# Kernel optimization log

Hardware: AMD Instinct MI355X
Metric: run time of the kernel (lower is better)

The kernel has to match this reference:

```python
import jax, jax.numpy as jnp
import numpy as np

NODE_DIM = 256
OUTPUT_DIM = 256
NUM_HOPS = 4
NUM_NODES = 25000
NUM_EDGES = 400000
NUM_TYPES = 10
FEAT_DIM = 32


def setup_inputs() -> dict:
    key = jax.random.key(0)
    ks = jax.random.split(key, 12)
    nodes = jax.random.normal(ks[0], (NUM_NODES, FEAT_DIM), dtype=jnp.float32)
    edges = jax.random.randint(ks[1], (2, NUM_EDGES), 0, NUM_NODES, dtype=jnp.int64)
    node_types = jax.random.randint(ks[2], (NUM_NODES,), 0, NUM_TYPES, dtype=jnp.int64)
    s = 0.02
    type_emb = jax.random.normal(ks[3], (NUM_TYPES, NODE_DIM), dtype=jnp.float32) * s
    W_proj = jax.random.normal(ks[4], (FEAT_DIM, NODE_DIM), dtype=jnp.float32) * s
    b_proj = jnp.zeros((NODE_DIM,), dtype=jnp.float32)
    W_msg = jax.random.normal(ks[5], (NUM_HOPS, 2 * NODE_DIM, NODE_DIM), dtype=jnp.float32) * s
    b_msg = jnp.zeros((NUM_HOPS, NODE_DIM), dtype=jnp.float32)
    W_upd = jax.random.normal(ks[6], (NUM_HOPS, 2 * NODE_DIM, NODE_DIM), dtype=jnp.float32) * s
    b_upd = jnp.zeros((NUM_HOPS, NODE_DIM), dtype=jnp.float32)
    W_out = jax.random.normal(ks[7], (NODE_DIM, OUTPUT_DIM), dtype=jnp.float32) * s
    b_out = jnp.zeros((OUTPUT_DIM,), dtype=jnp.float32)
    return {"nodes": nodes, "edges": edges, "node_types": node_types,
            "type_emb": type_emb, "W_proj": W_proj, "b_proj": b_proj,
            "W_msg": W_msg, "b_msg": b_msg, "W_upd": W_upd, "b_upd": b_upd,
            "W_out": W_out, "b_out": b_out}


def reference(nodes, edges, node_types, type_emb, W_proj, b_proj,
              W_msg, b_msg, W_upd, b_upd, W_out, b_out):
    n = nodes.shape[0]
    src, dst = edges[0], edges[1]
    # initial node states: linear proj + type embedding
    h = nodes @ W_proj + b_proj + type_emb[node_types]  # [N, D]
    for i in range(NUM_HOPS):
        edge_feat = jnp.concatenate([h[src], h[dst]], axis=1)      # [E, 2D]
        messages = edge_feat @ W_msg[i] + b_msg[i]                 # [E, D]
        agg = jax.ops.segment_sum(messages, dst, num_segments=n)   # [N, D]
        h = jax.nn.relu(jnp.concatenate([h, agg], axis=1) @ W_upd[i] + b_upd[i])
    graph_embedding = jnp.max(h, axis=0)                           # [D]
    return graph_embedding @ W_out + b_out                          # [output_dim]
```

## Files before the change

kernel.cpp:

```cpp
#include <hip/hip_runtime.h>
#include <hip/hip_bf16.h>

#define NDIM 256
#define FDIM 32
#define HOPS 4
#define NPB 8

typedef __attribute__((ext_vector_type(8))) short short8;
typedef __attribute__((ext_vector_type(4))) float f32x4;
typedef __attribute__((ext_vector_type(2))) float f32x2;

__device__ inline float b2f(unsigned short u) {
    union { unsigned int i; float f; } v; v.i = ((unsigned int)u) << 16; return v.f;
}
__device__ inline unsigned short f2b(float f) {
    union { float f; unsigned int i; } v; v.f = f;
    unsigned int r = v.i + 0x7FFF + ((v.i >> 16) & 1);
    return (unsigned short)(r >> 16);
}
__device__ inline unsigned char f2fp8(float v) {
    return (unsigned char)(__builtin_amdgcn_cvt_pk_fp8_f32(v, v, 0, false) & 0xFF);
}

__global__ __launch_bounds__(256) void prep_mega_kernel(
        const int* __restrict__ dst, int* __restrict__ deg, int E, int histB,
        const float* __restrict__ Wm, const float* __restrict__ Wu,
        const float* __restrict__ bm,
        unsigned short* __restrict__ WtA, unsigned short* __restrict__ WtB,
        unsigned short* __restrict__ WtC,
        float* __restrict__ cvec, int* __restrict__ geInt,
        unsigned char* __restrict__ h8row,
        const float* __restrict__ nodes, const int* __restrict__ node_types,
        const float* __restrict__ type_emb, const float* __restrict__ W_proj,
        const float* __restrict__ b_proj,
        unsigned short* __restrict__ h, unsigned char* __restrict__ h8, int n) {
    __shared__ float T[32][33];
    __shared__ float Af[32][68];
    __shared__ float Bf[32][68];
    __shared__ float sb[256];
    int b = blockIdx.x;
    int t = threadIdx.x;

    if (b < histB) {
        int e = b * 256 + t;
        if (e < E) atomicAdd(&deg[dst[e]], 1);
    } else if (b < histB + 389) {
        int bb = b - histB;
        if (bb < 256) {
            int hop = bb >> 6;
            int rem = bb & 63;
            int k0 = (rem & 7) * 32, n0 = (rem >> 3) * 32;
            const float* src = Wu + (size_t)hop * 512 * 256;
            unsigned short* dstp = WtB + (size_t)hop * 256 * 256;
            int tr = t >> 5, tc = t & 31;
#pragma unroll
            for (int r = 0; r < 4; ++r) {
                int k = tr + r * 8;
                T[tc][k] = src[(size_t)(k0 + k) * 256 + n0 + tc];
            }
            __syncthreads();
#pragma unroll
            for (int r = 0; r < 4; ++r) {
                int nn = tr + r * 8;
                dstp[(size_t)(n0 + nn) * 256 + k0 + tc] = f2b(T[nn][tc]);
            }
        } else if (bb < 384) {
            int idx = bb - 256;
            int m = idx >> 4;
            int rem = idx & 15;
            int k0 = (rem & 3) * 64, n0 = (rem >> 2) * 64;
            int hop = m >> 1, which = m & 1;
            const float* A = Wm + (size_t)hop * 512 * 256 + (size_t)which * 256 * 256;
            const float* B = Wu + (size_t)hop * 512 * 256 + (size_t)256 * 256;
            unsigned short* W = (which ? WtC : WtA) + (size_t)hop * 256 * 256;
            int tx = t & 15, ty = t >> 4;
            float acc[4][4];
#pragma unroll
            for (int a = 0; a < 4; ++a)
#pragma unroll
                for (int c = 0; c < 4; ++c) acc[a][c] = 0.f;

            for (int j0 = 0; j0 < 256; j0 += 32) {
                __syncthreads();
#pragma unroll
                for (int c = 0; c < 2; ++c) {
                    int idx2 = t + c * 256;
                    int kk = idx2 >> 3;
                    int jj = (idx2 & 7) * 4;
                    float4 va = *(const float4*)&A[(size_t)(k0 + kk) * 256 + j0 + jj];
                    Af[jj + 0][kk] = va.x; Af[jj + 1][kk] = va.y;
                    Af[jj + 2][kk] = va.z; Af[jj + 3][kk] = va.w;
                    int jj2 = idx2 >> 4;
                    int nn = (idx2 & 15) * 4;
                    float4 vb = *(const float4*)&B[(size_t)(j0 + jj2) * 256 + n0 + nn];
                    *(float4*)&Bf[jj2][nn] = vb;
                }
                __syncthreads();
#pragma unroll
                for (int jj = 0; jj < 32; ++jj) {
                    float av[4];
#pragma unroll
                    for (int a = 0; a < 4; ++a) av[a] = Af[jj][ty * 4 + a];
                    float4 bv = *(const float4*)&Bf[jj][tx * 4];
#pragma unroll
                    for (int a = 0; a < 4; ++a) {
                        acc[a][0] += av[a] * bv.x; acc[a][1] += av[a] * bv.y;
                        acc[a][2] += av[a] * bv.z; acc[a][3] += av[a] * bv.w;
                    }
                }
            }
#pragma unroll
            for (int c = 0; c < 4; ++c) {
                int nn = n0 + tx * 4 + c;
                ushort4 o;
                o.x = f2b(acc[0][c]); o.y = f2b(acc[1][c]);
                o.z = f2b(acc[2][c]); o.w = f2b(acc[3][c]);
                *(ushort4*)&W[(size_t)nn * 256 + k0 + ty * 4] = o;
            }
        } else if (bb < 388) {
            int hop = bb - 384;
            sb[t] = bm[hop * 256 + t];
            __syncthreads();
            const float* B = Wu + (size_t)hop * 512 * 256 + (size_t)256 * 256;
            float acc = 0.f;
#pragma unroll 8
            for (int j = 0; j < 256; ++j) acc += sb[j] * B[(size_t)j * 256 + t];
            cvec[hop * 256 + t] = acc;
        } else {
            geInt[t] = 0;
            h8row[t] = 0;
        }
    } else {
        int v0 = (b - histB - 389) * NPB;
        {
            int j = t >> 5, f = t & 31;
            int v = v0 + j;
            sb[t] = (v < n) ? nodes[(size_t)v * FDIM + f] : 0.f;
        }
        __syncthreads();
        float acc[NPB];
#pragma unroll
        for (int j = 0; j < NPB; ++j) {
            int v = v0 + j;
            acc[j] = (v < n) ? (b_proj[t] + type_emb[(size_t)node_types[v] * NDIM + t]) : 0.f;
        }
#pragma unroll 4
        for (int k = 0; k < FDIM; ++k) {
            float wv = W_proj[(size_t)k * NDIM + t];
#pragma unroll
            for (int j = 0; j < NPB; ++j)
                acc[j] += sb[j * FDIM + k] * wv;
        }
#pragma unroll
        for (int j = 0; j < NPB; ++j) {
            int v = v0 + j;
            if (v < n) {
                h[(size_t)v * NDIM + t] = f2b(acc[j]);
                h8[(size_t)v * NDIM + t] = f2fp8(acc[j]);
            }
        }
    }
}

__global__ __launch_bounds__(1024) void scan_kernel(const int* __restrict__ deg,
                                                    int* __restrict__ rowptr,
                                                    int* __restrict__ cursor, int n) {
    __shared__ int wsum[16];
    int t = threadIdx.x;
    int per4 = (n + 4095) >> 12;
    int base = t * per4 * 4;
    int4 v4[8];
#pragma unroll 8
    for (int j = 0; j < per4; ++j) {
        int4 d = *(const int4*)(deg + base + j * 4);
        d.x = (d.x + 7) & ~7; d.y = (d.y + 7) & ~7;
        d.z = (d.z + 7) & ~7; d.w = (d.w + 7) & ~7;
        v4[j] = d;
    }
    int s = 0;
#pragma unroll 8
    for (int j = 0; j < per4; ++j) s += v4[j].x + v4[j].y + v4[j].z + v4[j].w;

    int lane = t & 63, wid = t >> 6;
    int v = s;
#pragma unroll
    for (int d = 1; d < 64; d <<= 1) {
        int u = __shfl_up(v, d, 64);
        if (lane >= d) v += u;
    }
    if (lane == 63) wsum[wid] = v;
    __syncthreads();
    if (wid == 0) {
        int ws = (lane < 16) ? wsum[lane] : 0;
#pragma unroll
        for (int d = 1; d < 16; d <<= 1) {
            int u = __shfl_up(ws, d, 64);
            if (lane >= d) ws += u;
        }
        if (lane < 16) wsum[lane] = ws;
    }
    __syncthreads();
    int run = (wid > 0 ? wsum[wid - 1] : 0) + (v - s);
#pragma unroll 8
    for (int j = 0; j < per4; ++j) {
        int idx = base + j * 4;
        int4 o;
        o.x = run; run += v4[j].x;
        o.y = run; run += v4[j].y;
        o.z = run; run += v4[j].z;
        o.w = run; run += v4[j].w;
        if (idx + 3 < n) {
            *(int4*)(rowptr + idx) = o;
            *(int4*)(cursor + idx) = o;
        } else if (idx < n) {
            const int* op = (const int*)&o;
            for (int e = 0; e < 4 && idx + e < n; ++e) {
                rowptr[idx + e] = op[e];
                cursor[idx + e] = op[e];
            }
        }
    }
    if (t == 1023) rowptr[n] = run;
}

__global__ void fillpad_kernel(const int* __restrict__ src, const int* __restrict__ dst,
                               int* __restrict__ cursor,
                               const int* __restrict__ rowptr, const int* __restrict__ deg,
                               int* __restrict__ col, int E, int fillB, int n) {
    int b = blockIdx.x;
    int t = threadIdx.x;
    if (b < fillB) {
        int e = b * 256 + t;
        if (e < E) {
            int d = dst[e];
            int p = atomicAdd(&cursor[d], 1);
            col[p] = src[e];
        }
    } else {
        int v = (b - fillB) * 256 + t;
        if (v < n) {
            int s = rowptr[v] + deg[v];
            int e0 = rowptr[v + 1];
            for (int i = s; i < e0; ++i) col[i] = n;
        }
    }
}

__global__ __launch_bounds__(256) void agg_kernel(const unsigned char* __restrict__ h8,
                                                  const int* __restrict__ rowptr,
                                                  const int* __restrict__ col,
                                                  unsigned short* __restrict__ S, int n) {
    int wave = threadIdx.x >> 6;
    int lane = threadIdx.x & 63;
    int half = lane >> 5;
    int hl = lane & 31;
    int v = blockIdx.x * 8 + wave * 2 + half;
    if (v >= n) return;
    int beg = rowptr[v], end = rowptr[v + 1];
    float a[8];
#pragma unroll
    for (int e = 0; e < 8; ++e) a[e] = 0.f;
    int cofs = hl * 8;
    for (int i = beg; i < end; i += 8) {
        int cc[8];
#pragma unroll
        for (int j = 0; j < 8; ++j) cc[j] = col[i + j];
        uint2 x[8];
#pragma unroll
        for (int j = 0; j < 8; ++j)
            x[j] = *(const uint2*)(h8 + (size_t)cc[j] * NDIM + cofs);
#pragma unroll
        for (int j = 0; j < 8; ++j) {
            f32x2 p0 = __builtin_amdgcn_cvt_pk_f32_fp8(x[j].x, false);
            f32x2 p1 = __builtin_amdgcn_cvt_pk_f32_fp8(x[j].x, true);
            f32x2 p2 = __builtin_amdgcn_cvt_pk_f32_fp8(x[j].y, false);
            f32x2 p3 = __builtin_amdgcn_cvt_pk_f32_fp8(x[j].y, true);
            a[0] += p0[0]; a[1] += p0[1]; a[2] += p1[0]; a[3] += p1[1];
            a[4] += p2[0]; a[5] += p2[1]; a[6] += p3[0]; a[7] += p3[1];
        }
    }
    uint4 o;
    unsigned short* op = (unsigned short*)&o;
#pragma unroll
    for (int e = 0; e < 8; ++e) op[e] = f2b(a[e]);
    *(uint4*)&S[(size_t)v * NDIM + cofs] = o;
}

#define BM 128
#define BN 64
#define BK 64
#define ASTR (BK + 8)

template <bool LAST>
__global__ __launch_bounds__(256) void gemm_hop_kernel(const unsigned short* __restrict__ S,
                                                       const unsigned short* __restrict__ hcur,
                                                       const int* __restrict__ deg,
                                                       const unsigned short* __restrict__ WtA,
                                                       const unsigned short* __restrict__ WtB,
                                                       const unsigned short* __restrict__ WtC,
                                                       const float* __restrict__ bupd,
                                                       const float* __restrict__ cvec,
                                                       unsigned short* __restrict__ Out,
                                                       unsigned char* __restrict__ Out8,
                                                       int* __restrict__ geInt, int n) {
    __shared__ unsigned short As[BM][ASTR];
    __shared__ unsigned short Bs[BN][ASTR];
    __shared__ unsigned short Cs[BN][ASTR];
    __shared__ int smax[BN];
    int t = threadIdx.x;
    int lane = t & 63;
    int w = t >> 6;
    int wm = w >> 1, wn = w & 1;
    int quad = lane >> 4, l16 = lane & 15;
    int row0 = blockIdx.x * BM;
    int n0 = blockIdx.y * BN;

    if (LAST) {
        if (t < BN) smax[t] = 0;
    }

    f32x4 acc1[4][2], acc2[4][2];
#pragma unroll
    for (int i = 0; i < 4; ++i)
#pragma unroll
        for (int j = 0; j < 2; ++j) { acc1[i][j] = (f32x4)(0.f); acc2[i][j] = (f32x4)(0.f); }

    for (int k0 = 0; k0 < NDIM; k0 += BK) {
        __syncthreads();
#pragma unroll
        for (int h2 = 0; h2 < 4; ++h2) {
            int c = t + h2 * 256;
            int r = c >> 3;
            int ko = (c & 7) * 8;
            int grow = row0 + r; if (grow >= n) grow = n - 1;
            *(uint4*)&As[r][ko] = *(const uint4*)(S + (size_t)grow * NDIM + k0 + ko);
        }
#pragma unroll
        for (int h2 = 0; h2 < 2; ++h2) {
            int c = t + h2 * 256;
            int r = c >> 3;
            int ko = (c & 7) * 8;
            *(uint4*)&Bs[r][ko] = *(const uint4*)(WtA + (size_t)(n0 + r) * NDIM + k0 + ko);
        }
        __syncthreads();
#pragma unroll
        for (int ks = 0; ks < BK; ks += 32) {
            short8 af[4], bf[2];
#pragma unroll
            for (int mt = 0; mt < 4; ++mt)
                af[mt] = *(const short8*)&As[wm * 64 + mt * 16 + l16][ks + quad * 8];
#pragma unroll
            for (int nt = 0; nt < 2; ++nt)
                bf[nt] = *(const short8*)&Bs[wn * 32 + nt * 16 + l16][ks + quad * 8];
#pragma unroll
            for (int mt = 0; mt < 4; ++mt)
#pragma unroll
                for (int nt = 0; nt < 2; ++nt)
                    acc1[mt][nt] = __builtin_amdgcn_mfma_f32_16x16x32_bf16(af[mt], bf[nt], acc1[mt][nt], 0, 0, 0);
        }
    }
    for (int k0 = 0; k0 < NDIM; k0 += BK) {
        __syncthreads();
#pragma unroll
        for (int h2 = 0; h2 < 4; ++h2) {
            int c = t + h2 * 256;
            int r = c >> 3;
            int ko = (c & 7) * 8;
            int grow = row0 + r; if (grow >= n) grow = n - 1;
            *(uint4*)&As[r][ko] = *(const uint4*)(hcur + (size_t)grow * NDIM + k0 + ko);
        }
#pragma unroll
        for (int h2 = 0; h2 < 2; ++h2) {
            int c = t + h2 * 256;
            int r = c >> 3;
            int ko = (c & 7) * 8;
            size_t widx = (size_t)(n0 + r) * NDIM + k0 + ko;
            *(uint4*)&Bs[r][ko] = *(const uint4*)(WtB + widx);
            *(uint4*)&Cs[r][ko] = *(const uint4*)(WtC + widx);
        }
        __syncthreads();
#pragma unroll
        for (int ks = 0; ks < BK; ks += 32) {
            short8 af[4], bf[2], cf[2];
#pragma unroll
            for (int mt = 0; mt < 4; ++mt)
                af[mt] = *(const short8*)&As[wm * 64 + mt * 16 + l16][ks + quad * 8];
#pragma unroll
            for (int nt = 0; nt < 2; ++nt) {
                bf[nt] = *(const short8*)&Bs[wn * 32 + nt * 16 + l16][ks + quad * 8];
                cf[nt] = *(const short8*)&Cs[wn * 32 + nt * 16 + l16][ks + quad * 8];
            }
#pragma unroll
            for (int mt = 0; mt < 4; ++mt)
#pragma unroll
                for (int nt = 0; nt < 2; ++nt) {
                    acc1[mt][nt] = __builtin_amdgcn_mfma_f32_16x16x32_bf16(af[mt], bf[nt], acc1[mt][nt], 0, 0, 0);
                    acc2[mt][nt] = __builtin_amdgcn_mfma_f32_16x16x32_bf16(af[mt], cf[nt], acc2[mt][nt], 0, 0, 0);
                }
        }
    }
#pragma unroll
    for (int mt = 0; mt < 4; ++mt) {
#pragma unroll
        for (int nt = 0; nt < 2; ++nt) {
            int lcol = wn * 32 + nt * 16 + l16;
            int col = n0 + lcol;
            float bu = bupd[col];
            float cv = cvec[col];
            float cmax = 0.f;
#pragma unroll
            for (int r = 0; r < 4; ++r) {
                int row = row0 + wm * 64 + mt * 16 + quad * 4 + r;
                if (row < n) {
                    float dg = (float)deg[row];
                    float v = fmaxf(acc1[mt][nt][r] + dg * (acc2[mt][nt][r] + cv) + bu, 0.f);
                    Out[(size_t)row * NDIM + col] = f2b(v);
                    if (!LAST) Out8[(size_t)row * NDIM + col] = f2fp8(v);
                    if (LAST) cmax = fmaxf(cmax, v);
                }
            }
            if (LAST) atomicMax(&smax[lcol], __float_as_int(cmax));
        }
    }
    if (LAST) {
        __syncthreads();
        if (t < BN) atomicMax(&geInt[n0 + t], smax[t]);
    }
}

__global__ __launch_bounds__(1024) void out_kernel(const float* __restrict__ ge,
                                                   const float* __restrict__ W_out,
                                                   const float* __restrict__ b_out,
                                                   float* __restrict__ out) {
    __shared__ float red[4][NDIM];
    int t = threadIdx.x & 255;
    int g = threadIdx.x >> 8;
    float acc = 0.f;
#pragma unroll 8
    for (int kk = 0; kk < 64; ++kk) {
        int k = g * 64 + kk;
        acc += ge[k] * W_out[k * NDIM + t];
    }
    red[g][t] = acc;
    __syncthreads();
    if (g == 0)
        out[t] = b_out[t] + red[0][t] + red[1][t] + red[2][t] + red[3][t];
}

extern "C" void kernel_launch(void* const* d_in, const int* in_sizes, int n_in,
                              void* d_out, int out_size, void* d_ws, size_t ws_size,
                              hipStream_t stream) {
    const float* nodes      = (const float*)d_in[0];
    const int*   edges      = (const int*)d_in[1];
    const int*   node_types = (const int*)d_in[2];
    const float* type_emb   = (const float*)d_in[3];
    const float* W_proj     = (const float*)d_in[4];
    const float* b_proj     = (const float*)d_in[5];
    const float* W_msg      = (const float*)d_in[6];
    const float* b_msg      = (const float*)d_in[7];
    const float* W_upd      = (const float*)d_in[8];
    const float* b_upd      = (const float*)d_in[9];
    const float* W_out      = (const float*)d_in[10];
    const float* b_out      = (const float*)d_in[11];

    int n = in_sizes[2];
    int E = in_sizes[1] / 2;
    const int* src = edges;
    const int* dst = edges + E;

    size_t off = 0;
    auto alloc = [&](size_t bytes) {
        void* p = (char*)d_ws + off;
        off += (bytes + 255) & ~(size_t)255;
        return p;
    };
    int* deg    = (int*)alloc((size_t)(n + 4096) * 4);
    int* rowptr = (int*)alloc((size_t)(n + 1) * 4);
    int* cursor = (int*)alloc((size_t)n * 4);
    int* col    = (int*)alloc((size_t)(E + 8 * n) * 4);
    unsigned short* WtA = (unsigned short*)alloc((size_t)HOPS * 256 * 256 * 2);
    unsigned short* WtB = (unsigned short*)alloc((size_t)HOPS * 256 * 256 * 2);
    unsigned short* WtC = (unsigned short*)alloc((size_t)HOPS * 256 * 256 * 2);
    float* cvec = (float*)alloc((size_t)HOPS * 256 * 4);
    int* geInt  = (int*)alloc((size_t)256 * 4);
    unsigned short* hA  = (unsigned short*)alloc((size_t)(n + 1) * NDIM * 2);
    unsigned short* hB  = (unsigned short*)alloc((size_t)(n + 1) * NDIM * 2);
    unsigned short* Sb  = (unsigned short*)alloc((size_t)n * NDIM * 2);
    unsigned char* h8   = (unsigned char*)alloc((size_t)(n + 1) * NDIM);

    hipMemsetAsync(deg, 0, (size_t)(n + 4096) * 4, stream);
    int eb = (E + 255) / 256;
    int pb = (n + 255) / 256;
    int ib = (n + NPB - 1) / NPB;
    prep_mega_kernel<<<eb + 389 + ib, 256, 0, stream>>>(
        dst, deg, E, eb,
        W_msg, W_upd, b_msg, WtA, WtB, WtC, cvec, geInt, h8 + (size_t)n * NDIM,
        nodes, node_types, type_emb, W_proj, b_proj, hA, h8, n);
    scan_kernel<<<1, 1024, 0, stream>>>(deg, rowptr, cursor, n);
    fillpad_kernel<<<eb + pb, 256, 0, stream>>>(src, dst, cursor, rowptr, deg, col, E, eb, n);

    unsigned short* h  = hA;
    unsigned short* ho = hB;
    int gx = (n + BM - 1) / BM;
    dim3 ggrid(gx, NDIM / BN);
    for (int i = 0; i < HOPS; ++i) {
        agg_kernel<<<(n + 7) / 8, 256, 0, stream>>>(h8, rowptr, col, Sb, n);
        size_t wofs = (size_t)i * 256 * 256;
        if (i == HOPS - 1)
            gemm_hop_kernel<true><<<ggrid, 256, 0, stream>>>(
                Sb, h, deg, WtA + wofs, WtB + wofs, WtC + wofs,
                b_upd + (size_t)i * NDIM, cvec + (size_t)i * NDIM, ho, h8, geInt, n);
        else
            gemm_hop_kernel<false><<<ggrid, 256, 0, stream>>>(
                Sb, h, deg, WtA + wofs, WtB + wofs, WtC + wofs,
                b_upd + (size_t)i * NDIM, cvec + (size_t)i * NDIM, ho, h8, geInt, n);
        unsigned short* tmp = h; h = ho; ho = tmp;
    }
    out_kernel<<<1, 1024, 0, stream>>>((const float*)geInt, W_out, b_out, (float*)d_out);
}
```

Measured before the change: 365.6 us.

## Move weight-product precompute to MFMA blocks in scan kernel, restructure aggregation

Removes the scalar FP32 tiled matmul that folds W_msg into W_upd from the prep kernel. It is recomputed with bf16 MFMA instructions in extra blocks of the scan kernel, which now launches 9 blocks, so the small weight GEMMs overlap the single-block scan instead of lengthening the prep kernel. The aggregation kernel is also restructured: each quarter-wave handles different neighbors with 16-byte fp8 loads per lane, and the partial sums are reduced with cross-lane shuffles. Converting the weight-product inputs to bf16 before multiplying adds rounding error compared with the FP32 accumulation.

```diff
diff --git a/kernel.cpp b/kernel.cpp
--- a/kernel.cpp
+++ b/kernel.cpp
@@ -24,10 +24,8 @@
 
 __global__ __launch_bounds__(256) void prep_mega_kernel(
         const int* __restrict__ dst, int* __restrict__ deg, int E, int histB,
-        const float* __restrict__ Wm, const float* __restrict__ Wu,
-        const float* __restrict__ bm,
-        unsigned short* __restrict__ WtA, unsigned short* __restrict__ WtB,
-        unsigned short* __restrict__ WtC,
+        const float* __restrict__ Wu, const float* __restrict__ bm,
+        unsigned short* __restrict__ WtB,
         float* __restrict__ cvec, int* __restrict__ geInt,
         unsigned char* __restrict__ h8row,
         const float* __restrict__ nodes, const int* __restrict__ node_types,
@@ -35,8 +33,6 @@
         const float* __restrict__ b_proj,
         unsigned short* __restrict__ h, unsigned char* __restrict__ h8, int n) {
     __shared__ float T[32][33];
-    __shared__ float Af[32][68];
-    __shared__ float Bf[32][68];
     __shared__ float sb[256];
     int b = blockIdx.x;
     int t = threadIdx.x;
@@ -44,7 +40,7 @@
     if (b < histB) {
         int e = b * 256 + t;
         if (e < E) atomicAdd(&deg[dst[e]], 1);
-    } else if (b < histB + 389) {
+    } else if (b < histB + 261) {
         int bb = b - histB;
         if (bb < 256) {
             int hop = bb >> 6;
@@ -64,61 +60,8 @@
                 int nn = tr + r * 8;
                 dstp[(size_t)(n0 + nn) * 256 + k0 + tc] = f2b(T[nn][tc]);
             }
-        } else if (bb < 384) {
-            int idx = bb - 256;
-            int m = idx >> 4;
-            int rem = idx & 15;
-            int k0 = (rem & 3) * 64, n0 = (rem >> 2) * 64;
-            int hop = m >> 1, which = m & 1;
-            const float* A = Wm + (size_t)hop * 512 * 256 + (size_t)which * 256 * 256;
-            const float* B = Wu + (size_t)hop * 512 * 256 + (size_t)256 * 256;
-            unsigned short* W = (which ? WtC : WtA) + (size_t)hop * 256 * 256;
-            int tx = t & 15, ty = t >> 4;
-            float acc[4][4];
-#pragma unroll
-            for (int a = 0; a < 4; ++a)
-#pragma unroll
-                for (int c = 0; c < 4; ++c) acc[a][c] = 0.f;
-
-            for (int j0 = 0; j0 < 256; j0 += 32) {
-                __syncthreads();
-#pragma unroll
-                for (int c = 0; c < 2; ++c) {
-                    int idx2 = t + c * 256;
-                    int kk = idx2 >> 3;
-                    int jj = (idx2 & 7) * 4;
-                    float4 va = *(const float4*)&A[(size_t)(k0 + kk) * 256 + j0 + jj];
-                    Af[jj + 0][kk] = va.x; Af[jj + 1][kk] = va.y;
-                    Af[jj + 2][kk] = va.z; Af[jj + 3][kk] = va.w;
-                    int jj2 = idx2 >> 4;
-                    int nn = (idx2 & 15) * 4;
-                    float4 vb = *(const float4*)&B[(size_t)(j0 + jj2) * 256 + n0 + nn];
-                    *(float4*)&Bf[jj2][nn] = vb;
-                }
-                __syncthreads();
-#pragma unroll
-                for (int jj = 0; jj < 32; ++jj) {
-                    float av[4];
-#pragma unroll
-                    for (int a = 0; a < 4; ++a) av[a] = Af[jj][ty * 4 + a];
-                    float4 bv = *(const float4*)&Bf[jj][tx * 4];
-#pragma unroll
-                    for (int a = 0; a < 4; ++a) {
-                        acc[a][0] += av[a] * bv.x; acc[a][1] += av[a] * bv.y;
-                        acc[a][2] += av[a] * bv.z; acc[a][3] += av[a] * bv.w;
-                    }
-                }
-            }
-#pragma unroll
-            for (int c = 0; c < 4; ++c) {
-                int nn = n0 + tx * 4 + c;
-                ushort4 o;
-                o.x = f2b(acc[0][c]); o.y = f2b(acc[1][c]);
-                o.z = f2b(acc[2][c]); o.w = f2b(acc[3][c]);
-                *(ushort4*)&W[(size_t)nn * 256 + k0 + ty * 4] = o;
-            }
-        } else if (bb < 388) {
-            int hop = bb - 384;
+        } else if (bb < 260) {
+            int hop = bb - 256;
             sb[t] = bm[hop * 256 + t];
             __syncthreads();
             const float* B = Wu + (size_t)hop * 512 * 256 + (size_t)256 * 256;
@@ -131,7 +74,7 @@
             h8row[t] = 0;
         }
     } else {
-        int v0 = (b - histB - 389) * NPB;
+        int v0 = (b - histB - 261) * NPB;
         {
             int j = t >> 5, f = t & 31;
             int v = v0 + j;
@@ -162,65 +105,125 @@
     }
 }
 
-__global__ __launch_bounds__(1024) void scan_kernel(const int* __restrict__ deg,
-                                                    int* __restrict__ rowptr,
-                                                    int* __restrict__ cursor, int n) {
+__global__ __launch_bounds__(1024) void scan_mm_kernel(
+        const int* __restrict__ deg, int* __restrict__ rowptr,
+        int* __restrict__ cursor, int n,
+        const float* __restrict__ Wm, const float* __restrict__ Wu,
+        unsigned short* __restrict__ WtA, unsigned short* __restrict__ WtC) {
     __shared__ int wsum[16];
     int t = threadIdx.x;
-    int per4 = (n + 4095) >> 12;
-    int base = t * per4 * 4;
-    int4 v4[8];
+    if (blockIdx.x == 0) {
+        int per4 = (n + 4095) >> 12;
+        int base = t * per4 * 4;
+        int4 v4[8];
 #pragma unroll 8
-    for (int j = 0; j < per4; ++j) {
-        int4 d = *(const int4*)(deg + base + j * 4);
-        d.x = (d.x + 7) & ~7; d.y = (d.y + 7) & ~7;
-        d.z = (d.z + 7) & ~7; d.w = (d.w + 7) & ~7;
-        v4[j] = d;
-    }
-    int s = 0;
+        for (int j = 0; j < per4; ++j) {
+            int4 d = *(const int4*)(deg + base + j * 4);
+            d.x = (d.x + 7) & ~7; d.y = (d.y + 7) & ~7;
+            d.z = (d.z + 7) & ~7; d.w = (d.w + 7) & ~7;
+            v4[j] = d;
+        }
+        int s = 0;
 #pragma unroll 8
-    for (int j = 0; j < per4; ++j) s += v4[j].x + v4[j].y + v4[j].z + v4[j].w;
-
-    int lane = t & 63, wid = t >> 6;
-    int v = s;
-#pragma unroll
-    for (int d = 1; d < 64; d <<= 1) {
-        int u = __shfl_up(v, d, 64);
-        if (lane >= d) v += u;
-    }
-    if (lane == 63) wsum[wid] = v;
-    __syncthreads();
-    if (wid == 0) {
-        int ws = (lane < 16) ? wsum[lane] : 0;
-#pragma unroll
-        for (int d = 1; d < 16; d <<= 1) {
-            int u = __shfl_up(ws, d, 64);
-            if (lane >= d) ws += u;
-        }
-        if (lane < 16) wsum[lane] = ws;
-    }
-    __syncthreads();
-    int run = (wid > 0 ? wsum[wid - 1] : 0) + (v - s);
+        for (int j = 0; j < per4; ++j) s += v4[j].x + v4[j].y + v4[j].z + v4[j].w;
+
+        int lane = t & 63, wid = t >> 6;
+        int v = s;
+#pragma unroll
+        for (int d = 1; d < 64; d <<= 1) {
+            int u = __shfl_up(v, d, 64);
+            if (lane >= d) v += u;
+        }
+        if (lane == 63) wsum[wid] = v;
+        __syncthreads();
+        if (wid == 0) {
+            int ws = (lane < 16) ? wsum[lane] : 0;
+#pragma unroll
+            for (int d = 1; d < 16; d <<= 1) {
+                int u = __shfl_up(ws, d, 64);
+                if (lane >= d) ws += u;
+            }
+            if (lane < 16) wsum[lane] = ws;
+        }
+        __syncthreads();
+        int run = (wid > 0 ? wsum[wid - 1] : 0) + (v - s);
 #pragma unroll 8
-    for (int j = 0; j < per4; ++j) {
-        int idx = base + j * 4;
-        int4 o;
-        o.x = run; run += v4[j].x;
-        o.y = run; run += v4[j].y;
-        o.z = run; run += v4[j].z;
-        o.w = run; run += v4[j].w;
-        if (idx + 3 < n) {
-            *(int4*)(rowptr + idx) = o;
-            *(int4*)(cursor + idx) = o;
-        } else if (idx < n) {
-            const int* op = (const int*)&o;
-            for (int e = 0; e < 4 && idx + e < n; ++e) {
-                rowptr[idx + e] = op[e];
-                cursor[idx + e] = op[e];
-            }
-        }
-    }
-    if (t == 1023) rowptr[n] = run;
+        for (int j = 0; j < per4; ++j) {
+            int idx = base + j * 4;
+            int4 o;
+            o.x = run; run += v4[j].x;
+            o.y = run; run += v4[j].y;
+            o.z = run; run += v4[j].z;
+            o.w = run; run += v4[j].w;
+            if (idx + 3 < n) {
+                *(int4*)(rowptr + idx) = o;
+                *(int4*)(cursor + idx) = o;
+            } else if (idx < n) {
+                const int* op = (const int*)&o;
+                for (int e = 0; e < 4 && idx + e < n; ++e) {
+                    rowptr[idx + e] = op[e];
+                    cursor[idx + e] = op[e];
+                }
+            }
+        }
+        if (t == 1023) rowptr[n] = run;
+        return;
+    }
+
+    int m = blockIdx.x - 1;
+    int hop = m >> 1, which = m & 1;
+    const float* A = Wm + (size_t)hop * 512 * 256 + (size_t)which * 256 * 256;
+    const float* B = Wu + (size_t)hop * 512 * 256 + (size_t)256 * 256;
+    unsigned short* W = (which ? WtC : WtA) + (size_t)hop * 256 * 256;
+    int wave = t >> 6, lane = t & 63;
+    int l16 = lane & 15, quad = lane >> 4;
+    int k0 = (wave & 3) * 64;
+    int n0 = (wave >> 2) * 64;
+    f32x4 acc[4][4];
+#pragma unroll
+    for (int i = 0; i < 4; ++i)
+#pragma unroll
+        for (int j = 0; j < 4; ++j) acc[i][j] = (f32x4)(0.f);
+
+    for (int j0 = 0; j0 < 256; j0 += 32) {
+        short8 af[4], bfr[4];
+#pragma unroll
+        for (int kt = 0; kt < 4; ++kt) {
+            const float* ap = A + (size_t)(k0 + kt * 16 + l16) * 256 + j0 + quad * 8;
+            float4 a0 = *(const float4*)ap;
+            float4 a1 = *(const float4*)(ap + 4);
+            short8 f;
+            f[0] = (short)f2b(a0.x); f[1] = (short)f2b(a0.y);
+            f[2] = (short)f2b(a0.z); f[3] = (short)f2b(a0.w);
+            f[4] = (short)f2b(a1.x); f[5] = (short)f2b(a1.y);
+            f[6] = (short)f2b(a1.z); f[7] = (short)f2b(a1.w);
+            af[kt] = f;
+        }
+#pragma unroll
+        for (int nt = 0; nt < 4; ++nt) {
+            const float* bp = B + (size_t)(j0 + quad * 8) * 256 + n0 + nt * 16 + l16;
+            short8 f;
+#pragma unroll
+            for (int i = 0; i < 8; ++i) f[i] = (short)f2b(bp[(size_t)i * 256]);
+            bfr[nt] = f;
+        }
+#pragma unroll
+        for (int kt = 0; kt < 4; ++kt)
+#pragma unroll
+            for (int nt = 0; nt < 4; ++nt)
+                acc[kt][nt] = __builtin_amdgcn_mfma_f32_16x16x32_bf16(af[kt], bfr[nt], acc[kt][nt], 0, 0, 0);
+    }
+#pragma unroll
+    for (int kt = 0; kt < 4; ++kt)
+#pragma unroll
+        for (int nt = 0; nt < 4; ++nt) {
+            int k = k0 + kt * 16 + quad * 4;
+            int nn = n0 + nt * 16 + l16;
+            ushort4 o;
+            o.x = f2b(acc[kt][nt][0]); o.y = f2b(acc[kt][nt][1]);
+            o.z = f2b(acc[kt][nt][2]); o.w = f2b(acc[kt][nt][3]);
+            *(ushort4*)&W[(size_t)nn * 256 + k] = o;
+        }
 }
 
 __global__ void fillpad_kernel(const int* __restrict__ src, const int* __restrict__ dst,
@@ -250,40 +253,56 @@
                                                   const int* __restrict__ rowptr,
                                                   const int* __restrict__ col,
                                                   unsigned short* __restrict__ S, int n) {
-    int wave = threadIdx.x >> 6;
-    int lane = threadIdx.x & 63;
-    int half = lane >> 5;
-    int hl = lane & 31;
-    int v = blockIdx.x * 8 + wave * 2 + half;
-    if (v >= n) return;
-    int beg = rowptr[v], end = rowptr[v + 1];
-    float a[8];
-#pragma unroll
-    for (int e = 0; e < 8; ++e) a[e] = 0.f;
-    int cofs = hl * 8;
-    for (int i = beg; i < end; i += 8) {
-        int cc[8];
-#pragma unroll
-        for (int j = 0; j < 8; ++j) cc[j] = col[i + j];
-        uint2 x[8];
-#pragma unroll
-        for (int j = 0; j < 8; ++j)
-            x[j] = *(const uint2*)(h8 + (size_t)cc[j] * NDIM + cofs);
-#pragma unroll
-        for (int j = 0; j < 8; ++j) {
-            f32x2 p0 = __builtin_amdgcn_cvt_pk_f32_fp8(x[j].x, false);
-            f32x2 p1 = __builtin_amdgcn_cvt_pk_f32_fp8(x[j].x, true);
-            f32x2 p2 = __builtin_amdgcn_cvt_pk_f32_fp8(x[j].y, false);
-            f32x2 p3 = __builtin_amdgcn_cvt_pk_f32_fp8(x[j].y, true);
-            a[0] += p0[0]; a[1] += p0[1]; a[2] += p1[0]; a[3] += p1[1];
-            a[4] += p2[0]; a[5] += p2[1]; a[6] += p3[0]; a[7] += p3[1];
-        }
-    }
-    uint4 o;
-    unsigned short* op = (unsigned short*)&o;
-#pragma unroll
-    for (int e = 0; e < 8; ++e) op[e] = f2b(a[e]);
-    *(uint4*)&S[(size_t)v * NDIM + cofs] = o;
+    int t = threadIdx.x;
+    int w = t >> 6, lane = t & 63;
+    int l16 = lane & 15, grp = lane >> 4;
+    int vbase = blockIdx.x * 8 + w * 2;
+    size_t cofs = (size_t)l16 * 16;
+#pragma unroll
+    for (int vi = 0; vi < 2; ++vi) {
+        int v = vbase + vi;
+        if (v >= n) continue;
+        int beg = rowptr[v], end = rowptr[v + 1];
+        float a[16];
+#pragma unroll
+        for (int c = 0; c < 16; ++c) a[c] = 0.f;
+        for (int i = beg; i < end; i += 8) {
+            int c0 = col[i + grp];
+            int c1 = col[i + 4 + grp];
+            uint4 x0 = *(const uint4*)(h8 + (size_t)c0 * NDIM + cofs);
+            uint4 x1 = *(const uint4*)(h8 + (size_t)c1 * NDIM + cofs);
+            const unsigned int* xp0 = (const unsigned int*)&x0;
+            const unsigned int* xp1 = (const unsigned int*)&x1;
+#pragma unroll
+            for (int q = 0; q < 4; ++q) {
+                f32x2 p0 = __builtin_amdgcn_cvt_pk_f32_fp8(xp0[q], false);
+                f32x2 p1 = __builtin_amdgcn_cvt_pk_f32_fp8(xp0[q], true);
+                f32x2 p2 = __builtin_amdgcn_cvt_pk_f32_fp8(xp1[q], false);
+                f32x2 p3 = __builtin_amdgcn_cvt_pk_f32_fp8(xp1[q], true);
+                a[q * 4 + 0] += p0[0] + p2[0];
+                a[q * 4 + 1] += p0[1] + p2[1];
+                a[q * 4 + 2] += p1[0] + p3[0];
+                a[q * 4 + 3] += p1[1] + p3[1];
+            }
+        }
+#pragma unroll
+        for (int c = 0; c < 16; ++c) {
+            a[c] += __shfl_xor(a[c], 16, 64);
+            a[c] += __shfl_xor(a[c], 32, 64);
+        }
+        if (grp == 0) {
+            ushort4 o0, o1, o2, o3;
+            o0.x = f2b(a[0]);  o0.y = f2b(a[1]);  o0.z = f2b(a[2]);  o0.w = f2b(a[3]);
+            o1.x = f2b(a[4]);  o1.y = f2b(a[5]);  o1.z = f2b(a[6]);  o1.w = f2b(a[7]);
+            o2.x = f2b(a[8]);  o2.y = f2b(a[9]);  o2.z = f2b(a[10]); o2.w = f2b(a[11]);
+            o3.x = f2b(a[12]); o3.y = f2b(a[13]); o3.z = f2b(a[14]); o3.w = f2b(a[15]);
+            unsigned short* sp = S + (size_t)v * NDIM + l16 * 16;
+            *(ushort4*)(sp + 0)  = o0;
+            *(ushort4*)(sp + 4)  = o1;
+            *(ushort4*)(sp + 8)  = o2;
+            *(ushort4*)(sp + 12) = o3;
+        }
+    }
 }
 
 #define BM 128
@@ -492,11 +511,11 @@
     int eb = (E + 255) / 256;
     int pb = (n + 255) / 256;
     int ib = (n + NPB - 1) / NPB;
-    prep_mega_kernel<<<eb + 389 + ib, 256, 0, stream>>>(
+    prep_mega_kernel<<<eb + 261 + ib, 256, 0, stream>>>(
         dst, deg, E, eb,
-        W_msg, W_upd, b_msg, WtA, WtB, WtC, cvec, geInt, h8 + (size_t)n * NDIM,
+        W_upd, b_msg, WtB, cvec, geInt, h8 + (size_t)n * NDIM,
         nodes, node_types, type_emb, W_proj, b_proj, hA, h8, n);
-    scan_kernel<<<1, 1024, 0, stream>>>(deg, rowptr, cursor, n);
+    scan_mm_kernel<<<9, 1024, 0, stream>>>(deg, rowptr, cursor, n, W_msg, W_upd, WtA, WtC);
     fillpad_kernel<<<eb + pb, 256, 0, stream>>>(src, dst, cursor, rowptr, deg, col, E, eb, n);
 
     unsigned short* h  = hA;
```

Result: slower. 414.7 us (+13.4%).
